# Kernel tuning notes

Hardware: AMD Instinct MI355X
Metric: run time of the kernel (lower is better)

## Reference

```python
import jax, jax.numpy as jnp
import numpy as np
from jax import lax

B, N, C = 8, 4096, 512
NH, R = 8, 8
HD = C // NH
EPS = 1e-3  # keras LayerNormalization default epsilon


def setup_inputs() -> dict:
    key = jax.random.key(0)
    ks = jax.random.split(key, 8)
    s = 0.02
    x = jax.random.normal(ks[0], (B, N, C), dtype=jnp.float32)
    Wq = jax.random.normal(ks[1], (C, C), dtype=jnp.float32) * s
    Wkv = jax.random.normal(ks[2], (C, 2 * C), dtype=jnp.float32) * s
    conv_w = jax.random.normal(ks[3], (R, R, C, C), dtype=jnp.float32) * s  # HWIO
    gamma = jnp.ones((C,), dtype=jnp.float32)
    beta = jnp.zeros((C,), dtype=jnp.float32)
    Wp = jax.random.normal(ks[4], (C, C), dtype=jnp.float32) * s
    bp = jnp.zeros((C,), dtype=jnp.float32)
    return {"x": x, "Wq": Wq, "Wkv": Wkv, "conv_w": conv_w,
            "gamma": gamma, "beta": beta, "Wp": Wp, "bp": bp}


def reference(x, Wq, Wkv, conv_w, gamma, beta, Wp, bp):
    b, n, c = x.shape
    h = w = int(np.sqrt(n))
    scale = 1.0 / np.sqrt(float(HD))

    # queries: Rearrange 'b n (hd nh) -> b n nh hd' then 'b n nh hd -> b nh n hd'
    q = x @ Wq                                   # [B, N, C]
    q = q.reshape(b, n, HD, NH).transpose(0, 3, 1, 2)  # [B, NH, N, HD]

    # spatial reduction of K/V: strided conv (SAME) + layernorm
    fmap = x.reshape(b, h, w, c)
    fmap = lax.conv_general_dilated(
        fmap, conv_w, window_strides=(R, R), padding="SAME",
        dimension_numbers=("NHWC", "HWIO", "NHWC"))   # [B, h/R, w/R, C]
    m = fmap.shape[1] * fmap.shape[2]
    fmap = fmap.reshape(b, m, c)
    mu = jnp.mean(fmap, axis=-1, keepdims=True)
    var = jnp.var(fmap, axis=-1, keepdims=True)
    fmap = (fmap - mu) * lax.rsqrt(var + EPS) * gamma + beta

    # key/value: Rearrange 'b m (f nh hd) -> b m f nh hd', perm [2,0,3,1,4]
    kv = fmap @ Wkv                              # [B, M, 2C]
    kv = kv.reshape(b, m, 2, NH, HD).transpose(2, 0, 3, 1, 4)  # [2, B, NH, M, HD]
    k, v = kv[0], kv[1]

    attn = jax.nn.softmax(jnp.einsum("bhnd,bhmd->bhnm", q, k) * scale, axis=-1)
    out = jnp.einsum("bhnm,bhmd->bhnd", attn, v)  # [B, NH, N, HD]
    out = out.transpose(0, 2, 1, 3).reshape(b, n, c)  # 'b n h c -> b n (h c)'
    return out @ Wp + bp
```

## Files before the change

kernel.cpp:

```cpp
#include <hip/hip_runtime.h>

typedef unsigned short u16;
typedef __bf16 bf16x8 __attribute__((ext_vector_type(8)));
typedef float floatx4 __attribute__((ext_vector_type(4)));

__device__ __forceinline__ u16 f2bf(float f) {
    unsigned u = __float_as_uint(f);
    u += 0x7fff + ((u >> 16) & 1);
    return (u16)(u >> 16);
}

#define GLOAD_LDS16(g, l) __builtin_amdgcn_global_load_lds( \
    (const __attribute__((address_space(1))) void*)(g),      \
    (__attribute__((address_space(3))) void*)(l), 16, 0, 0)

__global__ __launch_bounds__(256) void prep_kernel(
    const float* __restrict__ x, u16* __restrict__ x_bf,
    const float* __restrict__ conv_w, u16* __restrict__ WconvT,
    const float* __restrict__ Wq, u16* __restrict__ WqTp,
    const float* __restrict__ Wp, u16* __restrict__ WpT,
    const float* __restrict__ Wkv, u16* __restrict__ WkvT)
{
    int blk = blockIdx.x;
    const int tid = threadIdx.x;
    if (blk < 16384) {
        size_t o = ((size_t)blk * 256 + tid) * 4;
        float4 v = *(const float4*)(x + o);
        unsigned w0 = (unsigned)f2bf(v.x) | ((unsigned)f2bf(v.y) << 16);
        unsigned w1 = (unsigned)f2bf(v.z) | ((unsigned)f2bf(v.w) << 16);
        *(uint2*)(x_bf + o) = make_uint2(w0, w1);
        return;
    }
    blk -= 16384;
    const float* in; u16* outp; int R, Cn, bx, by; bool perm = false;
    if (blk < 16384)      { in = conv_w; outp = WconvT; R = 32768; Cn = 512;  bx = blk & 15; by = blk >> 4; }
    else if (blk < 16640) { blk -= 16384; in = Wq;  outp = WqTp; R = 512; Cn = 512;  bx = blk & 15; by = blk >> 4; perm = true; }
    else if (blk < 16896) { blk -= 16640; in = Wp;  outp = WpT;  R = 512; Cn = 512;  bx = blk & 15; by = blk >> 4; }
    else                  { blk -= 16896; in = Wkv; outp = WkvT; R = 512; Cn = 1024; bx = blk & 31; by = blk >> 5; }
    __shared__ float tile[32][33];
    const int c0 = bx * 32, r0 = by * 32;
    const int tx = tid & 31, ty = tid >> 5;
    #pragma unroll
    for (int yy = 0; yy < 4; ++yy)
        tile[ty + yy * 8][tx] = in[(size_t)(r0 + ty + yy * 8) * Cn + c0 + tx];
    __syncthreads();
    #pragma unroll
    for (int yy = 0; yy < 4; ++yy) {
        int cc = c0 + ty + yy * 8;
        int np = perm ? ((cc & 7) * 64 + (cc >> 3)) : cc;
        outp[(size_t)np * R + r0 + tx] = f2bf(tile[tx][ty + yy * 8]);
    }
}

template<int MODE, int ASRC>
__global__ __launch_bounds__(256) void gemm_bt(
    const u16* __restrict__ A, const u16* __restrict__ B, float* __restrict__ out,
    int M, int N, int K, int KC, const float* __restrict__ bias)
{
    __shared__ u16 As[2][128 * 32];
    __shared__ u16 Bs[2][128 * 32];
    const int tid = threadIdx.x;
    const int wv = tid >> 6, lane = tid & 63;
    const int quad = lane >> 4, l15 = lane & 15;
    const int bm = blockIdx.y * 128, bn = blockIdx.x * 128;
    const int k0 = blockIdx.z * KC;
    const int wr = wv >> 1, wc = wv & 1;

    floatx4 acc[4][4];
    #pragma unroll
    for (int i = 0; i < 4; ++i)
        #pragma unroll
        for (int j = 0; j < 4; ++j)
            acc[i][j] = (floatx4){0.f, 0.f, 0.f, 0.f};

    for (int kt = 0; kt < KC; kt += 64) {
        const int kk = k0 + kt;
        #pragma unroll
        for (int hf = 0; hf < 2; ++hf) {
            #pragma unroll
            for (int c2 = 0; c2 < 2; ++c2) {
                int idx = ((wv * 2 + c2) * 64 + lane) * 8;
                int row = idx >> 5, col = idx & 31;
                int k = kk + hf * 32 + col;
                if (ASRC == 0) {
                    const u16* ga = A + (size_t)(bm + row) * K + k;
                    GLOAD_LDS16(ga, &As[hf][(wv * 2 + c2) * 512]);
                } else {
                    int p = bm + row;
                    int b = p >> 6, ij = p & 63, ii = ij >> 3, jj = ij & 7;
                    int r12 = k >> 9, r1 = r12 >> 3, r2 = r12 & 7;
                    int n = (ii * 8 + r1) * 64 + jj * 8 + r2;
                    const u16* ga = A + ((size_t)(b * 4096 + n)) * 512 + (k & 511);
                    GLOAD_LDS16(ga, &As[hf][(wv * 2 + c2) * 512]);
                }
                const u16* gb = B + (size_t)(bn + row) * K + k;
                GLOAD_LDS16(gb, &Bs[hf][(wv * 2 + c2) * 512]);
            }
        }
        __syncthreads();
        #pragma unroll
        for (int ks = 0; ks < 2; ++ks) {
            bf16x8 af[4], bfr[4];
            #pragma unroll
            for (int i = 0; i < 4; ++i)
                af[i] = *(const bf16x8*)&As[ks][(wr * 64 + i * 16 + l15) * 32 + quad * 8];
            #pragma unroll
            for (int j = 0; j < 4; ++j)
                bfr[j] = *(const bf16x8*)&Bs[ks][(wc * 64 + j * 16 + l15) * 32 + quad * 8];
            #pragma unroll
            for (int i = 0; i < 4; ++i)
                #pragma unroll
                for (int j = 0; j < 4; ++j)
                    acc[i][j] = __builtin_amdgcn_mfma_f32_16x16x32_bf16(af[i], bfr[j], acc[i][j], 0, 0, 0);
        }
        __syncthreads();
    }

    #pragma unroll
    for (int i = 0; i < 4; ++i) {
        #pragma unroll
        for (int j = 0; j < 4; ++j) {
            #pragma unroll
            for (int r = 0; r < 4; ++r) {
                int m = bm + wr * 64 + i * 16 + quad * 4 + r;
                int n = bn + wc * 64 + j * 16 + l15;
                float v = acc[i][j][r];
                if (MODE == 0) {
                    ((u16*)out)[(size_t)blockIdx.z * 262144 + (size_t)m * N + n] = f2bf(v);
                } else if (MODE == 1) {
                    int b = m >> 12, nn = m & 4095;
                    int h = n >> 6, d = n & 63;
                    ((u16*)out)[((size_t)((b * 8 + h) * 4096 + nn)) * 64 + d] = f2bf(v);
                } else if (MODE == 2) {
                    int b = m >> 6, mm = m & 63;
                    int f = n >> 9, c = n & 511, h = c >> 6, d = c & 63;
                    size_t idx;
                    if (f == 0) idx = ((size_t)((b * 8 + h) * 64 + mm)) * 64 + d;
                    else        idx = 262144 + ((size_t)((b * 8 + h) * 64 + d)) * 64 + mm;
                    out[idx] = v;
                } else {
                    out[(size_t)m * 512 + n] = v + bias[n];
                }
            }
        }
    }
}

__global__ __launch_bounds__(256) void reduce_ln_bf16(
    const u16* __restrict__ part, u16* __restrict__ out,
    const float* __restrict__ gamma, const float* __restrict__ beta)
{
    int row = blockIdx.x, tid = threadIdx.x;
    const unsigned* base = (const unsigned*)(part + (size_t)row * 512) + tid;
    float2 v = {0.f, 0.f};
    #pragma unroll 8
    for (int z = 0; z < 64; ++z) {
        unsigned u = base[(size_t)z * 131072];
        v.x += __uint_as_float(u << 16);
        v.y += __uint_as_float(u & 0xffff0000u);
    }
    float s = v.x + v.y, ss = v.x * v.x + v.y * v.y;
    #pragma unroll
    for (int off = 32; off > 0; off >>= 1) {
        s  += __shfl_down(s, off);
        ss += __shfl_down(ss, off);
    }
    __shared__ float red[8];
    __shared__ float stats[2];
    int wvi = tid >> 6, lane = tid & 63;
    if (lane == 0) { red[wvi * 2] = s; red[wvi * 2 + 1] = ss; }
    __syncthreads();
    if (tid == 0) {
        float S = red[0] + red[2] + red[4] + red[6];
        float SS = red[1] + red[3] + red[5] + red[7];
        float mean = S * (1.f / 512.f);
        float var = SS * (1.f / 512.f) - mean * mean;
        stats[0] = mean; stats[1] = rsqrtf(var + 1e-3f);
    }
    __syncthreads();
    float mean = stats[0], rstd = stats[1];
    float o0 = (v.x - mean) * rstd * gamma[tid * 2]     + beta[tid * 2];
    float o1 = (v.y - mean) * rstd * gamma[tid * 2 + 1] + beta[tid * 2 + 1];
    unsigned w = (unsigned)f2bf(o0) | ((unsigned)f2bf(o1) << 16);
    *(unsigned*)&out[(size_t)row * 512 + tid * 2] = w;
}

__global__ __launch_bounds__(256) void attn_mfma(
    const u16* __restrict__ qbf, const float* __restrict__ kvf, u16* __restrict__ attn_out)
{
    __shared__ u16 Ksh[64 * 64];
    __shared__ u16 Vt[64 * 64];
    __shared__ u16 Psh[4][32 * 64];
    const int bh = blockIdx.x, qt = blockIdx.y;
    const int tid = threadIdx.x;
    const int wv = tid >> 6, lane = tid & 63;
    const int quad = lane >> 4, l15 = lane & 15;

    {
        const float* kb = kvf + (size_t)bh * 4096;
        const float* vb = kvf + 262144 + (size_t)bh * 4096;
        for (int t = tid; t < 2048; t += 256) {
            float2 a = ((const float2*)kb)[t];
            ((unsigned*)Ksh)[t] = (unsigned)f2bf(a.x) | ((unsigned)f2bf(a.y) << 16);
            float2 b2 = ((const float2*)vb)[t];
            ((unsigned*)Vt)[t] = (unsigned)f2bf(b2.x) | ((unsigned)f2bf(b2.y) << 16);
        }
    }
    __syncthreads();

    const u16* qb = qbf + ((size_t)bh * 4096 + qt * 128 + wv * 32) * 64;
    bf16x8 qf[2][2];
    #pragma unroll
    for (int i = 0; i < 2; ++i)
        #pragma unroll
        for (int ks = 0; ks < 2; ++ks)
            qf[i][ks] = *(const bf16x8*)(qb + (i * 16 + l15) * 64 + ks * 32 + quad * 8);

    floatx4 s[2][4];
    #pragma unroll
    for (int i = 0; i < 2; ++i)
        #pragma unroll
        for (int j = 0; j < 4; ++j)
            s[i][j] = (floatx4){0.f, 0.f, 0.f, 0.f};
    #pragma unroll
    for (int j = 0; j < 4; ++j) {
        #pragma unroll
        for (int ks = 0; ks < 2; ++ks) {
            bf16x8 kf = *(const bf16x8*)&Ksh[(j * 16 + l15) * 64 + ks * 32 + quad * 8];
            #pragma unroll
            for (int i = 0; i < 2; ++i)
                s[i][j] = __builtin_amdgcn_mfma_f32_16x16x32_bf16(qf[i][ks], kf, s[i][j], 0, 0, 0);
        }
    }

    u16* P = Psh[wv];
    float rs[2][4];
    #pragma unroll
    for (int i = 0; i < 2; ++i)
        #pragma unroll
        for (int r = 0; r < 4; ++r) rs[i][r] = 0.f;
    #pragma unroll
    for (int i = 0; i < 2; ++i)
        #pragma unroll
        for (int j = 0; j < 4; ++j)
            #pragma unroll
            for (int r = 0; r < 4; ++r) {
                float e = __expf(s[i][j][r] * 0.125f);
                rs[i][r] += e;
                P[(i * 16 + quad * 4 + r) * 64 + j * 16 + l15] = f2bf(e);
            }
    #pragma unroll
    for (int m = 1; m < 16; m <<= 1)
        #pragma unroll
        for (int i = 0; i < 2; ++i)
            #pragma unroll
            for (int r = 0; r < 4; ++r)
                rs[i][r] += __shfl_xor(rs[i][r], m);
    __syncthreads();

    floatx4 o[2][4];
    #pragma unroll
    for (int i = 0; i < 2; ++i)
        #pragma unroll
        for (int j = 0; j < 4; ++j)
            o[i][j] = (floatx4){0.f, 0.f, 0.f, 0.f};
    #pragma unroll
    for (int ks = 0; ks < 2; ++ks) {
        bf16x8 pf[2];
        #pragma unroll
        for (int i = 0; i < 2; ++i)
            pf[i] = *(const bf16x8*)&P[(i * 16 + l15) * 64 + ks * 32 + quad * 8];
        #pragma unroll
        for (int j = 0; j < 4; ++j) {
            bf16x8 vf = *(const bf16x8*)&Vt[(j * 16 + l15) * 64 + ks * 32 + quad * 8];
            #pragma unroll
            for (int i = 0; i < 2; ++i)
                o[i][j] = __builtin_amdgcn_mfma_f32_16x16x32_bf16(pf[i], vf, o[i][j], 0, 0, 0);
        }
    }

    const int b = bh >> 3, h = bh & 7;
    #pragma unroll
    for (int i = 0; i < 2; ++i) {
        #pragma unroll
        for (int r = 0; r < 4; ++r) {
            float inv = 1.f / rs[i][r];
            int n = qt * 128 + wv * 32 + i * 16 + quad * 4 + r;
            u16* op = attn_out + ((size_t)(b * 4096 + n)) * 512 + h * 64;
            #pragma unroll
            for (int j = 0; j < 4; ++j)
                op[j * 16 + l15] = f2bf(o[i][j][r] * inv);
        }
    }
}

extern "C" void kernel_launch(void* const* d_in, const int* in_sizes, int n_in,
                              void* d_out, int out_size, void* d_ws, size_t ws_size,
                              hipStream_t stream) {
    const float* x      = (const float*)d_in[0];
    const float* Wq     = (const float*)d_in[1];
    const float* Wkv    = (const float*)d_in[2];
    const float* conv_w = (const float*)d_in[3];
    const float* gamma  = (const float*)d_in[4];
    const float* beta   = (const float*)d_in[5];
    const float* Wp     = (const float*)d_in[6];
    const float* bp     = (const float*)d_in[7];
    float* out = (float*)d_out;

    char* w = (char*)d_ws;
    const size_t MB = 1ull << 20;
    u16*   x_bf      = (u16*)(w + 0);
    u16*   WconvT    = (u16*)(w + 32 * MB);
    u16*   WqTp      = (u16*)(w + 64 * MB);
    u16*   WkvT      = (u16*)(w + 65 * MB);
    u16*   WpT       = (u16*)(w + 66 * MB);
    u16*   q_bf      = (u16*)(w + 67 * MB);
    u16*   fmap_part = (u16*)(w + 99 * MB);
    u16*   fmap_ln   = (u16*)(w + 131 * MB);
    float* kv_f      = (float*)(w + 132 * MB);
    u16*   attn_bf   = (u16*)(w + 134 * MB);

    prep_kernel<<<33792, 256, 0, stream>>>(x, x_bf, conv_w, WconvT, Wq, WqTp, Wp, WpT, Wkv, WkvT);

    gemm_bt<1, 0><<<dim3(4, 256, 1), 256, 0, stream>>>(x_bf, WqTp, (float*)q_bf, 32768, 512, 512, 512, nullptr);
    gemm_bt<0, 1><<<dim3(4, 4, 64), 256, 0, stream>>>(x_bf, WconvT, (float*)fmap_part, 512, 512, 32768, 512, nullptr);
    reduce_ln_bf16<<<512, 256, 0, stream>>>(fmap_part, fmap_ln, gamma, beta);
    gemm_bt<2, 0><<<dim3(8, 4, 1), 256, 0, stream>>>(fmap_ln, WkvT, kv_f, 512, 1024, 512, 512, nullptr);
    attn_mfma<<<dim3(64, 32), 256, 0, stream>>>(q_bf, kv_f, attn_bf);
    gemm_bt<3, 0><<<dim3(4, 256, 1), 256, 0, stream>>>(attn_bf, WpT, out, 32768, 512, 512, 512, bp);
}
```

Before: 333.1 us.

## Rewrite conv weight transpose with vectorized bf16 tiles and halve conv split-K

The conv weight transpose-to-bf16 moves out of the generic 32x32 float tile path into a dedicated path. Each block reads 128x64 float4 chunks, stores bf16 into shared memory, and writes packed 32-bit pairs, so it uses fewer blocks and wider global accesses. The conv GEMM's split-K factor drops from 64 to 32 with a larger K chunk, and the LayerNorm reduction now sums 32 partial slices instead of 64. This cuts partial-sum traffic and reduction work, but leaves only 512 blocks for the conv GEMM, which may lower occupancy.

```diff
diff --git a/kernel.cpp b/kernel.cpp
--- a/kernel.cpp
+++ b/kernel.cpp
@@ -32,12 +32,39 @@
         return;
     }
     blk -= 16384;
+
+    __shared__ __align__(16) char smem[16896];
+
+    if (blk < 2048) {
+        u16 (*T)[66] = (u16(*)[66])smem;
+        const int by = blk >> 8;
+        const int bx = blk & 255;
+        const int c0 = by * 64, k0 = bx * 128;
+        const int f = tid & 15, kl = tid >> 4;
+        #pragma unroll
+        for (int it = 0; it < 8; ++it) {
+            int k = kl + it * 16;
+            float4 v = *(const float4*)(conv_w + (size_t)(k0 + k) * 512 + c0 + f * 4);
+            *(unsigned*)&T[k][f * 4]     = (unsigned)f2bf(v.x) | ((unsigned)f2bf(v.y) << 16);
+            *(unsigned*)&T[k][f * 4 + 2] = (unsigned)f2bf(v.z) | ((unsigned)f2bf(v.w) << 16);
+        }
+        __syncthreads();
+        const int cl = tid >> 6, p = tid & 63;
+        #pragma unroll
+        for (int it = 0; it < 16; ++it) {
+            int c = cl + it * 4;
+            unsigned lo = T[p * 2][c], hi = T[p * 2 + 1][c];
+            *(unsigned*)&WconvT[(size_t)(c0 + c) * 32768 + k0 + p * 2] = lo | (hi << 16);
+        }
+        return;
+    }
+    blk -= 2048;
+
     const float* in; u16* outp; int R, Cn, bx, by; bool perm = false;
-    if (blk < 16384)      { in = conv_w; outp = WconvT; R = 32768; Cn = 512;  bx = blk & 15; by = blk >> 4; }
-    else if (blk < 16640) { blk -= 16384; in = Wq;  outp = WqTp; R = 512; Cn = 512;  bx = blk & 15; by = blk >> 4; perm = true; }
-    else if (blk < 16896) { blk -= 16640; in = Wp;  outp = WpT;  R = 512; Cn = 512;  bx = blk & 15; by = blk >> 4; }
-    else                  { blk -= 16896; in = Wkv; outp = WkvT; R = 512; Cn = 1024; bx = blk & 31; by = blk >> 5; }
-    __shared__ float tile[32][33];
+    if (blk < 256)      { in = Wq;  outp = WqTp; R = 512; Cn = 512;  bx = blk & 15; by = blk >> 4; perm = true; }
+    else if (blk < 512) { blk -= 256; in = Wp;  outp = WpT;  R = 512; Cn = 512;  bx = blk & 15; by = blk >> 4; }
+    else                { blk -= 512; in = Wkv; outp = WkvT; R = 512; Cn = 1024; bx = blk & 31; by = blk >> 5; }
+    float (*tile)[33] = (float(*)[33])smem;
     const int c0 = bx * 32, r0 = by * 32;
     const int tx = tid & 31, ty = tid >> 5;
     #pragma unroll
@@ -154,7 +181,7 @@
     const unsigned* base = (const unsigned*)(part + (size_t)row * 512) + tid;
     float2 v = {0.f, 0.f};
     #pragma unroll 8
-    for (int z = 0; z < 64; ++z) {
+    for (int z = 0; z < 32; ++z) {
         unsigned u = base[(size_t)z * 131072];
         v.x += __uint_as_float(u << 16);
         v.y += __uint_as_float(u & 0xffff0000u);
@@ -320,10 +347,10 @@
     float* kv_f      = (float*)(w + 132 * MB);
     u16*   attn_bf   = (u16*)(w + 134 * MB);
 
-    prep_kernel<<<33792, 256, 0, stream>>>(x, x_bf, conv_w, WconvT, Wq, WqTp, Wp, WpT, Wkv, WkvT);
+    prep_kernel<<<19456, 256, 0, stream>>>(x, x_bf, conv_w, WconvT, Wq, WqTp, Wp, WpT, Wkv, WkvT);
 
     gemm_bt<1, 0><<<dim3(4, 256, 1), 256, 0, stream>>>(x_bf, WqTp, (float*)q_bf, 32768, 512, 512, 512, nullptr);
-    gemm_bt<0, 1><<<dim3(4, 4, 64), 256, 0, stream>>>(x_bf, WconvT, (float*)fmap_part, 512, 512, 32768, 512, nullptr);
+    gemm_bt<0, 1><<<dim3(4, 4, 32), 256, 0, stream>>>(x_bf, WconvT, (float*)fmap_part, 512, 512, 32768, 1024, nullptr);
     reduce_ln_bf16<<<512, 256, 0, stream>>>(fmap_part, fmap_ln, gamma, beta);
     gemm_bt<2, 0><<<dim3(8, 4, 1), 256, 0, stream>>>(fmap_ln, WkvT, kv_f, 512, 1024, 512, 512, nullptr);
     attn_mfma<<<dim3(64, 32), 256, 0, stream>>>(q_bf, kv_f, attn_bf);
```

Measured after the change: 327.7 us. No clear change (-1.6%).
